# Performance work log

Hardware: AMD Instinct MI355X
Metric: run time of the kernel (lower is better)

The kernel has to match this reference:

```python
import jax, jax.numpy as jnp
import numpy as np

N = 1048576
NUM_LEVELS = 16; LEVEL_DIM = 2; BASE_RES = 16; TABLE = 1 << 19
BOUND = 1.0; DESIRED = 64
_s = np.exp(np.log(DESIRED / BASE_RES) / (NUM_LEVELS - 1))
RESOLUTIONS = [int(np.floor(BASE_RES * _s ** l)) for l in range(NUM_LEVELS)]
OFFS = np.array([[(i >> 0) & 1, (i >> 1) & 1, (i >> 2) & 1] for i in range(8)], dtype=np.int32)
PRIMES = (1, 2654435761, 805459861)


def _corner_index(corner, R):
    # corner: [N,8,3] int32 in [0,R]. Dense index if grid fits in table, else spatial hash.
    if (R + 1) ** 3 <= TABLE:
        stride = jnp.array([1, R + 1, (R + 1) ** 2], dtype=jnp.int32)
        return jnp.sum(corner * stride, axis=-1)
    c = corner.astype(jnp.uint32)
    h = (c[..., 0] * jnp.uint32(PRIMES[0])) ^ (c[..., 1] * jnp.uint32(PRIMES[1])) ^ (c[..., 2] * jnp.uint32(PRIMES[2]))
    return (h % jnp.uint32(TABLE)).astype(jnp.int32)


def hashgrid_encode(x, embeddings):
    # x: [N,3] in [-BOUND,BOUND]; embeddings: [L, TABLE, C]
    pos = (x + BOUND) / (2.0 * BOUND)  # [0,1]
    offs = jnp.asarray(OFFS)  # [8,3]
    outs = []
    for l, R in enumerate(RESOLUTIONS):  # fixed small loop over levels
        xg = pos * R
        x0 = jnp.clip(jnp.floor(xg).astype(jnp.int32), 0, R - 1)  # [N,3]
        f = xg - x0.astype(xg.dtype)  # trilinear fractions [N,3]
        corners = x0[:, None, :] + offs[None]  # [N,8,3]
        idx = _corner_index(corners, R)  # [N,8]
        feats = embeddings[l][idx]  # [N,8,C] irregular gather
        w = jnp.prod(jnp.where(offs[None] == 1, f[:, None, :], 1.0 - f[:, None, :]), axis=-1)  # [N,8]
        outs.append(jnp.sum(feats * w[..., None], axis=1))  # [N,C]
    return jnp.concatenate(outs, axis=-1)  # [N, L*C] = [N,32]


def sh_encode(d):
    # degree-4 real spherical harmonics (16 coeffs), torch-ngp convention
    x, y, z = d[..., 0], d[..., 1], d[..., 2]
    xx, yy, zz = x * x, y * y, z * z
    xy, yz, xz = x * y, y * z, x * z
    return jnp.stack([
        0.28209479177387814 * jnp.ones_like(x),
        -0.48860251190291987 * y,
        0.48860251190291987 * z,
        -0.48860251190291987 * x,
        1.0925484305920792 * xy,
        -1.0925484305920792 * yz,
        0.94617469575755997 * zz - 0.31539156525252005,
        -1.0925484305920792 * xz,
        0.54627421529603959 * (xx - yy),
        0.59004358992664352 * y * (yy - 3.0 * xx),
        2.8906114426405538 * xy * z,
        0.45704579946446572 * y * (1.0 - 5.0 * zz),
        0.3731763325901154 * z * (5.0 * zz - 3.0),
        0.45704579946446572 * x * (1.0 - 5.0 * zz),
        1.4453057213202769 * z * (xx - yy),
        0.59004358992664352 * x * (3.0 * yy - xx),
    ], axis=-1)  # [N,16]


def setup_inputs() -> dict:
    key = jax.random.key(0)
    ks = jax.random.split(key, 8)
    x = jax.random.uniform(ks[0], (N, 3), jnp.float32) * 2.0 - 1.0  # in [-bound, bound]
    d_raw = jax.random.normal(ks[1], (N, 3), jnp.float32)
    d = d_raw / (jnp.linalg.norm(d_raw, axis=-1, keepdims=True) + 1e-8)  # unit view dirs
    embeddings = jax.random.normal(ks[2], (NUM_LEVELS, TABLE, LEVEL_DIM), jnp.float32) * 1e-2
    def w(k, i, o):
        return jax.random.normal(k, (i, o), jnp.float32) / np.sqrt(i).astype(np.float32)
    ws0 = w(ks[3], 32, 64)
    ws1 = w(ks[4], 64, 16)
    wc0 = w(ks[5], 31, 64)
    wc1 = w(ks[6], 64, 64)
    wc2 = w(ks[7], 64, 1)
    return {"x": x, "d": d, "embeddings": embeddings,
            "ws0": ws0, "ws1": ws1, "wc0": wc0, "wc1": wc1, "wc2": wc2}


def reference(x, d, embeddings, ws0, ws1, wc0, wc1, wc2):
    # sigma branch: hashgrid encode -> 2-layer bias-free MLP
    h = hashgrid_encode(x, embeddings)          # [N,32]
    h = jax.nn.relu(h @ ws0) @ ws1              # [N,16]
    sigma = jnp.abs(h[:, :1])                   # [N,1]
    geo_feat = h[:, 1:]                         # [N,15]
    # color branch: SH encode dir, concat geo feature, 3-layer bias-free MLP
    hd = jnp.concatenate([sh_encode(d), geo_feat], axis=-1)  # [N,31]
    c = jax.nn.relu(hd @ wc0)
    c = jax.nn.relu(c @ wc1)
    color = jnp.abs(c @ wc2)                    # [N,1]
    return sigma, color
```

## Files before the change

### kernel.cpp

```cpp
#include <hip/hip_runtime.h>
#include <cmath>

#define NPTS 1048576
#define TABLE_SZ 524288
#define NBUCK 32768

typedef _Float16 half8 __attribute__((ext_vector_type(8)));
typedef _Float16 half4 __attribute__((ext_vector_type(4)));
typedef _Float16 h2 __attribute__((ext_vector_type(2)));
typedef __fp16 fp16x2 __attribute__((ext_vector_type(2)));
typedef float floatx4 __attribute__((ext_vector_type(4)));
typedef unsigned int uint2a4 __attribute__((ext_vector_type(2), aligned(4)));

#define MFMA16x16x32 __builtin_amdgcn_mfma_f32_16x16x32_f16

__device__ __forceinline__ h2 as_h2(unsigned int u) {
    union { unsigned int u; h2 h; } c; c.u = u; return c.h;
}
__device__ __forceinline__ unsigned int pk_u32(float a, float b) {
    union { fp16x2 h; unsigned int u; } c;
    c.h = __builtin_amdgcn_cvt_pkrtz(a, b);
    return c.u;
}

__global__ void prepack_weights(const float* __restrict__ ws0,
                                const float* __restrict__ ws1,
                                const float* __restrict__ wc0,
                                const float* __restrict__ wc1,
                                const float* __restrict__ wc2,
                                half8* __restrict__ wfrag)
{
    const int f = blockIdx.x, l = threadIdx.x;
    const int lane_m = l & 15, k0 = (l >> 4) * 8;
    half8 hv;

    if (f >= 6 && f < 10) {
        const int m = 16*(f-6) + lane_m;
        #pragma unroll
        for (int e = 0; e < 8; ++e) {
            const int k = k0 + e;
            float v;
            if (k < 16)       v = wc0[k*64 + m];
            else if (k == 16) v = 0.0f;
            else              v = wc0[(k-1)*64 + m];
            hv[e] = (_Float16)v;
        }
        wfrag[f*64 + l] = hv;
        return;
    }

    const float* W; int Kreal, Mreal, mt, kt;
    if (f < 4)       { W = ws0; Kreal = 32; Mreal = 64; mt = f;          kt = 0;        }
    else if (f < 6)  { W = ws1; Kreal = 64; Mreal = 16; mt = 0;          kt = f - 4;    }
    else if (f < 18) { W = wc1; Kreal = 64; Mreal = 64; mt = (f-10)>>1;  kt = (f-10)&1; }
    else             { W = wc2; Kreal = 64; Mreal = 1;  mt = 0;          kt = f - 18;   }

    const int m  = 16*mt + lane_m;
    const int kk0 = 32*kt + k0;
    #pragma unroll
    for (int e = 0; e < 8; ++e) {
        const int k = kk0 + e;
        const float v = (m < Mreal && k < Kreal) ? W[k*Mreal + m] : 0.0f;
        hv[e] = (_Float16)v;
    }
    wfrag[f*64 + l] = hv;
}

__global__ __launch_bounds__(256) void convert_tables(
    const float* __restrict__ emb, unsigned int* __restrict__ tabu,
    unsigned int* __restrict__ hist, int zero_hist,
    int4 ra, int4 rb, int4 rc, int4 rd,
    int4 oa, int4 ob, int4 oc, int4 od)
{
    const int l = blockIdx.y;
    if (l == 16) {
        if (zero_hist) {
            const int e = blockIdx.x * 256 + threadIdx.x;
            if (e < NBUCK) hist[e] = 0u;
        }
        return;
    }
    const int q = l >> 2, j = l & 3;
    const int4 rv = (q == 0) ? ra : (q == 1) ? rb : (q == 2) ? rc : rd;
    const int4 ov = (q == 0) ? oa : (q == 1) ? ob : (q == 2) ? oc : od;
    const int R   = (j == 0) ? rv.x : (j == 1) ? rv.y : (j == 2) ? rv.z : rv.w;
    const int off = (j == 0) ? ov.x : (j == 1) ? ov.y : (j == 2) ? ov.z : ov.w;
    const int n = (R+1)*(R+1)*(R+1);
    const int e = blockIdx.x * 256 + threadIdx.x;
    if (e >= n) return;
    const float2 v = *(const float2*)(emb + (size_t)l * (TABLE_SZ*2) + 2*(size_t)e);
    tabu[off + e] = pk_u32(v.x, v.y);
}

__device__ __forceinline__ int bucket_of(float px, float py, float pz) {
    int bx = (int)(px * 32.0f); bx = bx < 0 ? 0 : (bx > 31 ? 31 : bx);
    int by = (int)(py * 32.0f); by = by < 0 ? 0 : (by > 31 ? 31 : by);
    int bz = (int)(pz * 32.0f); bz = bz < 0 ? 0 : (bz > 31 ? 31 : bz);
    return bx | (by << 5) | (bz << 10);
}

__global__ __launch_bounds__(256) void hist_kernel(
    const float* __restrict__ xin, unsigned int* __restrict__ hist,
    unsigned int* __restrict__ rnk)
{
    const int i = blockIdx.x * 256 + threadIdx.x;
    const float px = (xin[3*i+0] + 1.0f) * 0.5f;
    const float py = (xin[3*i+1] + 1.0f) * 0.5f;
    const float pz = (xin[3*i+2] + 1.0f) * 0.5f;
    rnk[i] = atomicAdd(&hist[bucket_of(px, py, pz)], 1u);
}

__global__ __launch_bounds__(1024) void scan_kernel(
    const unsigned int* __restrict__ hist, unsigned int* __restrict__ off)
{
    __shared__ unsigned int ssum[1024];
    const int t = threadIdx.x;
    unsigned int v[32];
    unsigned int s = 0;
    #pragma unroll
    for (int j = 0; j < 32; ++j) {
        const unsigned int h = hist[t*32 + j];
        v[j] = s; s += h;
    }
    ssum[t] = s;
    __syncthreads();
    for (int d = 1; d < 1024; d <<= 1) {
        const unsigned int add = (t >= d) ? ssum[t-d] : 0u;
        __syncthreads();
        ssum[t] += add;
        __syncthreads();
    }
    const unsigned int base = (t == 0) ? 0u : ssum[t-1];
    #pragma unroll
    for (int j = 0; j < 32; ++j) off[t*32 + j] = base + v[j];
}

__global__ __launch_bounds__(256) void scatter_pd(
    const float* __restrict__ xin, const float* __restrict__ din,
    const unsigned int* __restrict__ boff, const unsigned int* __restrict__ rnk,
    float4* __restrict__ pd)
{
    const int i = blockIdx.x * 256 + threadIdx.x;
    const float px = (xin[3*i+0] + 1.0f) * 0.5f;
    const float py = (xin[3*i+1] + 1.0f) * 0.5f;
    const float pz = (xin[3*i+2] + 1.0f) * 0.5f;
    const int b = bucket_of(px, py, pz);
    const unsigned int pos = boff[b] + rnk[i];
    const float dx = din[3*i+0], dy = din[3*i+1], dz = din[3*i+2];
    pd[2*(size_t)pos]     = make_float4(px, py, pz, 0.0f);
    pd[2*(size_t)pos + 1] = make_float4(dx, dy, dz, __uint_as_float((unsigned int)i));
}

__global__ __launch_bounds__(256, 4) void ngp_gather_sorted(
    const float4* __restrict__ pd, const unsigned int* __restrict__ tabu,
    _Float16* __restrict__ feats,
    int4 ra, int4 rb, int4 rc, int4 rd,
    int4 oa, int4 ob, int4 oc, int4 od)
{
    const int p = blockIdx.x * 256 + threadIdx.x;
    const int q = blockIdx.y;

    const float4 xv = pd[2*(size_t)p];
    const float px = xv.x, py = xv.y, pz = xv.z;

    const int4 rv = (q == 0) ? ra : (q == 1) ? rb : (q == 2) ? rc : rd;
    const int4 ov = (q == 0) ? oa : (q == 1) ? ob : (q == 2) ? oc : od;

    uint2a4 P[16];
    float fx[4], fy[4], fz[4];

    #pragma unroll
    for (int j = 0; j < 4; ++j) {
        const int R   = (j == 0) ? rv.x : (j == 1) ? rv.y : (j == 2) ? rv.z : rv.w;
        const int off = (j == 0) ? ov.x : (j == 1) ? ov.y : (j == 2) ? ov.z : ov.w;
        const float Rf = (float)R;
        const float gx = px*Rf, gy = py*Rf, gz = pz*Rf;
        int x0 = (int)floorf(gx); x0 = x0 < 0 ? 0 : (x0 > R-1 ? R-1 : x0);
        int y0 = (int)floorf(gy); y0 = y0 < 0 ? 0 : (y0 > R-1 ? R-1 : y0);
        int z0 = (int)floorf(gz); z0 = z0 < 0 ? 0 : (z0 > R-1 ? R-1 : z0);
        fx[j] = gx - (float)x0; fy[j] = gy - (float)y0; fz[j] = gz - (float)z0;
        const int s1 = R + 1, s2 = s1 * s1;
        const unsigned int* tab = tabu + off;
        const int b = x0 + y0*s1 + z0*s2;
        P[4*j+0] = *(const uint2a4*)(tab + b);
        P[4*j+1] = *(const uint2a4*)(tab + b + s1);
        P[4*j+2] = *(const uint2a4*)(tab + b + s2);
        P[4*j+3] = *(const uint2a4*)(tab + b + s1 + s2);
    }

    union { half8 v; h2 h[4]; } hv;
    #pragma unroll
    for (int j = 0; j < 4; ++j) {
        const _Float16 fxh = (_Float16)fx[j];
        const _Float16 fyh = (_Float16)fy[j];
        const _Float16 fzh = (_Float16)fz[j];
        const h2 fx2 = {fxh, fxh}, fy2 = {fyh, fyh}, fz2 = {fzh, fzh};
        const h2 c000 = as_h2(P[4*j+0].x), c100 = as_h2(P[4*j+0].y);
        const h2 c010 = as_h2(P[4*j+1].x), c110 = as_h2(P[4*j+1].y);
        const h2 c001 = as_h2(P[4*j+2].x), c101 = as_h2(P[4*j+2].y);
        const h2 c011 = as_h2(P[4*j+3].x), c111 = as_h2(P[4*j+3].y);
        const h2 a00 = c000 + fx2 * (c100 - c000);
        const h2 a10 = c010 + fx2 * (c110 - c010);
        const h2 a01 = c001 + fx2 * (c101 - c001);
        const h2 a11 = c011 + fx2 * (c111 - c011);
        const h2 b0  = a00 + fy2 * (a10 - a00);
        const h2 b1  = a01 + fy2 * (a11 - a01);
        hv.h[j] = b0 + fz2 * (b1 - b0);
    }
    *(half8*)&feats[((size_t)q * NPTS + p) * 8] = hv.v;
}

__global__ __launch_bounds__(256, 4) void ngp_gather_lin(
    const float* __restrict__ xin, const unsigned int* __restrict__ tabu,
    _Float16* __restrict__ feats,
    int4 ra, int4 rb, int4 rc, int4 rd,
    int4 oa, int4 ob, int4 oc, int4 od)
{
    const int tid = blockIdx.x * 256 + threadIdx.x;
    const int p = tid >> 2;
    const int q = tid & 3;

    const float px = (xin[3*p+0] + 1.0f) * 0.5f;
    const float py = (xin[3*p+1] + 1.0f) * 0.5f;
    const float pz = (xin[3*p+2] + 1.0f) * 0.5f;

    const int4 rv = (q == 0) ? ra : (q == 1) ? rb : (q == 2) ? rc : rd;
    const int4 ov = (q == 0) ? oa : (q == 1) ? ob : (q == 2) ? oc : od;

    uint2a4 P[16];
    float fx[4], fy[4], fz[4];
    #pragma unroll
    for (int j = 0; j < 4; ++j) {
        const int R   = (j == 0) ? rv.x : (j == 1) ? rv.y : (j == 2) ? rv.z : rv.w;
        const int off = (j == 0) ? ov.x : (j == 1) ? ov.y : (j == 2) ? ov.z : ov.w;
        const float Rf = (float)R;
        const float gx = px*Rf, gy = py*Rf, gz = pz*Rf;
        int x0 = (int)floorf(gx); x0 = x0 < 0 ? 0 : (x0 > R-1 ? R-1 : x0);
        int y0 = (int)floorf(gy); y0 = y0 < 0 ? 0 : (y0 > R-1 ? R-1 : y0);
        int z0 = (int)floorf(gz); z0 = z0 < 0 ? 0 : (z0 > R-1 ? R-1 : z0);
        fx[j] = gx - (float)x0; fy[j] = gy - (float)y0; fz[j] = gz - (float)z0;
        const int s1 = R + 1, s2 = s1 * s1;
        const unsigned int* tab = tabu + off;
        const int b = x0 + y0*s1 + z0*s2;
        P[4*j+0] = *(const uint2a4*)(tab + b);
        P[4*j+1] = *(const uint2a4*)(tab + b + s1);
        P[4*j+2] = *(const uint2a4*)(tab + b + s2);
        P[4*j+3] = *(const uint2a4*)(tab + b + s1 + s2);
    }
    union { half8 v; h2 h[4]; } hv;
    #pragma unroll
    for (int j = 0; j < 4; ++j) {
        const _Float16 fxh = (_Float16)fx[j];
        const _Float16 fyh = (_Float16)fy[j];
        const _Float16 fzh = (_Float16)fz[j];
        const h2 fx2 = {fxh, fxh}, fy2 = {fyh, fyh}, fz2 = {fzh, fzh};
        const h2 c000 = as_h2(P[4*j+0].x), c100 = as_h2(P[4*j+0].y);
        const h2 c010 = as_h2(P[4*j+1].x), c110 = as_h2(P[4*j+1].y);
        const h2 c001 = as_h2(P[4*j+2].x), c101 = as_h2(P[4*j+2].y);
        const h2 c011 = as_h2(P[4*j+3].x), c111 = as_h2(P[4*j+3].y);
        const h2 a00 = c000 + fx2 * (c100 - c000);
        const h2 a10 = c010 + fx2 * (c110 - c010);
        const h2 a01 = c001 + fx2 * (c101 - c001);
        const h2 a11 = c011 + fx2 * (c111 - c011);
        const h2 b0  = a00 + fy2 * (a10 - a00);
        const h2 b1  = a01 + fy2 * (a11 - a01);
        hv.h[j] = b0 + fz2 * (b1 - b0);
    }
    *(half8*)&feats[(size_t)p*32 + q*8] = hv.v;
}

template<int MODE>
__global__ __launch_bounds__(256) void ngp_mlp(
    const float* __restrict__ din, const _Float16* __restrict__ feats,
    const float4* __restrict__ pd,
    const half8* __restrict__ wfrag, float* __restrict__ out)
{
    __shared__ __align__(16) _Float16 smM[4][64][72];

    const int tid  = threadIdx.x;
    const int w    = tid >> 6, lane = tid & 63;
    const int gbase = (blockIdx.x * 4 + w) * 64;

    const int n = lane & 15, g = lane >> 4;
    const floatx4 zz = {0.f, 0.f, 0.f, 0.f};

    unsigned int orig[4];
    float dX[4], dY[4], dZ[4];
    #pragma unroll
    for (int nt = 0; nt < 4; ++nt) {
        const int pt = nt*16 + n;
        if (MODE == 2) {
            const float4 dv = pd[2*(size_t)(gbase + pt) + 1];
            dX[nt] = dv.x; dY[nt] = dv.y; dZ[nt] = dv.z;
            orig[nt] = __float_as_uint(dv.w);
        } else {
            orig[nt] = gbase + pt;
            dX[nt] = din[3*orig[nt]+0]; dY[nt] = din[3*orig[nt]+1]; dZ[nt] = din[3*orig[nt]+2];
        }
    }

    auto storeQ = [&](int pt, int mt, floatx4 a) {
        union { unsigned int u[2]; half4 v; } c;
        c.u[0] = pk_u32(fmaxf(a[0], 0.f), fmaxf(a[1], 0.f));
        c.u[1] = pk_u32(fmaxf(a[2], 0.f), fmaxf(a[3], 0.f));
        *(half4*)&smM[w][pt][16*mt + 4*g] = c.v;
    };

    {
        const half8 A0 = wfrag[0*64+lane], A1 = wfrag[1*64+lane];
        const half8 A2 = wfrag[2*64+lane], A3 = wfrag[3*64+lane];
        #pragma unroll
        for (int nt = 0; nt < 4; ++nt) {
            const int pt = nt*16 + n;
            half8 B;
            if (MODE == 2)
                B = *(const half8*)&feats[((size_t)g * NPTS + (gbase + pt)) * 8];
            else
                B = *(const half8*)&feats[(size_t)(gbase + pt)*32 + 8*g];
            floatx4 a0 = MFMA16x16x32(A0, B, zz, 0,0,0);
            floatx4 a1 = MFMA16x16x32(A1, B, zz, 0,0,0);
            floatx4 a2 = MFMA16x16x32(A2, B, zz, 0,0,0);
            floatx4 a3 = MFMA16x16x32(A3, B, zz, 0,0,0);
            storeQ(pt, 0, a0); storeQ(pt, 1, a1); storeQ(pt, 2, a2); storeQ(pt, 3, a3);
        }
    }
    asm volatile("" ::: "memory");

    unsigned int s1a[4], s1b[4];
    {
        const half8 A0 = wfrag[4*64+lane], A1 = wfrag[5*64+lane];
        #pragma unroll
        for (int nt = 0; nt < 4; ++nt) {
            const int pt = nt*16 + n;
            const half8 B0 = *(const half8*)&smM[w][pt][ 0 + 8*g];
            const half8 B1 = *(const half8*)&smM[w][pt][32 + 8*g];
            floatx4 acc = MFMA16x16x32(A0, B0, zz, 0,0,0);
            acc = MFMA16x16x32(A1, B1, acc, 0,0,0);
            s1a[nt] = pk_u32(acc[0], acc[1]);
            s1b[nt] = pk_u32(acc[2], acc[3]);
            if (g == 0) out[orig[nt]] = fabsf(acc[0]);
        }
    }
    asm volatile("" ::: "memory");

    {
        const half8 A0 = wfrag[6*64+lane], A1 = wfrag[7*64+lane];
        const half8 A2 = wfrag[8*64+lane], A3 = wfrag[9*64+lane];
        const int srcA = ((g & 1) << 5) + n;
        #pragma unroll
        for (int nt = 0; nt < 4; ++nt) {
            const int pt = nt*16 + n;
            const unsigned int w0 = __shfl(s1a[nt], srcA);
            const unsigned int w1 = __shfl(s1b[nt], srcA);
            const unsigned int w2 = __shfl(s1a[nt], srcA + 16);
            const unsigned int w3 = __shfl(s1b[nt], srcA + 16);
            union { half8 v; unsigned int u[4]; } B;
            if (g < 2) {
                const float x = dX[nt], y = dY[nt], z = dZ[nt];
                const float xx = x*x, yy = y*y, zzq = z*z;
                const float xy = x*y, yz = y*z, xz = x*z;
                float s[8];
                if (g == 0) {
                    s[0] = 0.28209479177387814f;
                    s[1] = -0.48860251190291987f * y;
                    s[2] =  0.48860251190291987f * z;
                    s[3] = -0.48860251190291987f * x;
                    s[4] =  1.0925484305920792f * xy;
                    s[5] = -1.0925484305920792f * yz;
                    s[6] =  0.94617469575756f * zzq - 0.31539156525252005f;
                    s[7] = -1.0925484305920792f * xz;
                } else {
                    s[0] =  0.5462742152960396f * (xx - yy);
                    s[1] =  0.5900435899266435f * y * (yy - 3.0f*xx);
                    s[2] =  2.890611442640554f * xy * z;
                    s[3] =  0.4570457994644657f * y * (1.0f - 5.0f*zzq);
                    s[4] =  0.3731763325901154f * z * (5.0f*zzq - 3.0f);
                    s[5] =  0.4570457994644657f * x * (1.0f - 5.0f*zzq);
                    s[6] =  1.445305721320277f * z * (xx - yy);
                    s[7] =  0.5900435899266435f * x * (3.0f*yy - xx);
                }
                B.u[0] = pk_u32(s[0], s[1]); B.u[1] = pk_u32(s[2], s[3]);
                B.u[2] = pk_u32(s[4], s[5]); B.u[3] = pk_u32(s[6], s[7]);
            } else {
                B.u[0] = w0; B.u[1] = w1; B.u[2] = w2; B.u[3] = w3;
            }
            floatx4 a0 = MFMA16x16x32(A0, B.v, zz, 0,0,0);
            floatx4 a1 = MFMA16x16x32(A1, B.v, zz, 0,0,0);
            floatx4 a2 = MFMA16x16x32(A2, B.v, zz, 0,0,0);
            floatx4 a3 = MFMA16x16x32(A3, B.v, zz, 0,0,0);
            storeQ(pt, 0, a0); storeQ(pt, 1, a1); storeQ(pt, 2, a2); storeQ(pt, 3, a3);
        }
    }
    asm volatile("" ::: "memory");

    {
        const half8 A0 = wfrag[10*64+lane], A1 = wfrag[11*64+lane];
        const half8 A2 = wfrag[12*64+lane], A3 = wfrag[13*64+lane];
        const half8 A4 = wfrag[14*64+lane], A5 = wfrag[15*64+lane];
        const half8 A6 = wfrag[16*64+lane], A7 = wfrag[17*64+lane];
        #pragma unroll
        for (int nt = 0; nt < 4; ++nt) {
            const int pt = nt*16 + n;
            const half8 B0 = *(const half8*)&smM[w][pt][ 0 + 8*g];
            const half8 B1 = *(const half8*)&smM[w][pt][32 + 8*g];
            floatx4 a0 = MFMA16x16x32(A0, B0, zz, 0,0,0); a0 = MFMA16x16x32(A1, B1, a0, 0,0,0);
            floatx4 a1 = MFMA16x16x32(A2, B0, zz, 0,0,0); a1 = MFMA16x16x32(A3, B1, a1, 0,0,0);
            floatx4 a2 = MFMA16x16x32(A4, B0, zz, 0,0,0); a2 = MFMA16x16x32(A5, B1, a2, 0,0,0);
            floatx4 a3 = MFMA16x16x32(A6, B0, zz, 0,0,0); a3 = MFMA16x16x32(A7, B1, a3, 0,0,0);
            storeQ(pt, 0, a0); storeQ(pt, 1, a1); storeQ(pt, 2, a2); storeQ(pt, 3, a3);
        }
    }
    asm volatile("" ::: "memory");

    {
        const half8 A0 = wfrag[18*64+lane], A1 = wfrag[19*64+lane];
        #pragma unroll
        for (int nt = 0; nt < 4; ++nt) {
            const int pt = nt*16 + n;
            const half8 B0 = *(const half8*)&smM[w][pt][ 0 + 8*g];
            const half8 B1 = *(const half8*)&smM[w][pt][32 + 8*g];
            floatx4 acc = MFMA16x16x32(A0, B0, zz, 0,0,0);
            acc = MFMA16x16x32(A1, B1, acc, 0,0,0);
            if (g == 0) out[NPTS + orig[nt]] = fabsf(acc[0]);
        }
    }
}

extern "C" void kernel_launch(void* const* d_in, const int* in_sizes, int n_in,
                              void* d_out, int out_size, void* d_ws, size_t ws_size,
                              hipStream_t stream)
{
    const float* x   = (const float*)d_in[0];
    const float* d   = (const float*)d_in[1];
    const float* emb = (const float*)d_in[2];
    const float* ws0 = (const float*)d_in[3];
    const float* ws1 = (const float*)d_in[4];
    const float* wc0 = (const float*)d_in[5];
    const float* wc1 = (const float*)d_in[6];
    const float* wc2 = (const float*)d_in[7];
    float* out = (float*)d_out;

    const size_t OFF_WFRAG = 0;
    const size_t OFF_TABU  = 32768;
    const size_t OFF_FEATS = OFF_TABU + 8388608;
    const size_t OFF_RNK   = OFF_FEATS;
    const size_t OFF_HIST  = OFF_FEATS + 67108864;
    const size_t OFF_BOFF  = OFF_HIST + NBUCK*4;
    const size_t OFF_PD    = OFF_BOFF + NBUCK*4;
    const size_t NEED_SORT = OFF_PD + (size_t)NPTS*32;
    const size_t NEED_LIN  = OFF_HIST;

    half8* wfrag        = (half8*)((char*)d_ws + OFF_WFRAG);
    unsigned int* tabu  = (unsigned int*)((char*)d_ws + OFF_TABU);
    _Float16* feats     = (_Float16*)((char*)d_ws + OFF_FEATS);
    unsigned int* rnk   = (unsigned int*)((char*)d_ws + OFF_RNK);
    unsigned int* hist  = (unsigned int*)((char*)d_ws + OFF_HIST);
    unsigned int* boff  = (unsigned int*)((char*)d_ws + OFF_BOFF);
    float4* pd          = (float4*)((char*)d_ws + OFF_PD);

    int r[16], off[16];
    const double s = std::exp(std::log(4.0) / 15.0);
    int acc = 0;
    for (int l = 0; l < 16; ++l) {
        r[l] = (int)std::floor(16.0 * std::pow(s, (double)l));
        off[l] = acc;
        acc += (r[l]+1)*(r[l]+1)*(r[l]+1);
    }
    const int4 ra = {r[0],  r[1],  r[2],  r[3]};
    const int4 rb = {r[4],  r[5],  r[6],  r[7]};
    const int4 rc = {r[8],  r[9],  r[10], r[11]};
    const int4 rd = {r[12], r[13], r[14], r[15]};
    const int4 oa = {off[0],  off[1],  off[2],  off[3]};
    const int4 ob = {off[4],  off[5],  off[6],  off[7]};
    const int4 oc = {off[8],  off[9],  off[10], off[11]};
    const int4 od = {off[12], off[13], off[14], off[15]};

    prepack_weights<<<20, 64, 0, stream>>>(ws0, ws1, wc0, wc1, wc2, wfrag);

    const int nmax = (r[15]+1)*(r[15]+1)*(r[15]+1);
    dim3 cgrid((nmax + 255) / 256, 17);

    if (ws_size >= NEED_SORT) {
        convert_tables<<<cgrid, 256, 0, stream>>>(emb, tabu, hist, 1, ra, rb, rc, rd, oa, ob, oc, od);
        hist_kernel<<<NPTS/256, 256, 0, stream>>>(x, hist, rnk);
        scan_kernel<<<1, 1024, 0, stream>>>(hist, boff);
        scatter_pd<<<NPTS/256, 256, 0, stream>>>(x, d, boff, rnk, pd);
        dim3 ggrid(NPTS/256, 4);
        ngp_gather_sorted<<<ggrid, 256, 0, stream>>>(pd, tabu, feats, ra, rb, rc, rd, oa, ob, oc, od);
        ngp_mlp<2><<<NPTS/256, 256, 0, stream>>>(d, feats, pd, wfrag, out);
    } else if (ws_size >= NEED_LIN) {
        convert_tables<<<cgrid, 256, 0, stream>>>(emb, tabu, hist, 0, ra, rb, rc, rd, oa, ob, oc, od);
        ngp_gather_lin<<<NPTS*4/256, 256, 0, stream>>>(x, tabu, feats, ra, rb, rc, rd, oa, ob, oc, od);
        ngp_mlp<0><<<NPTS/256, 256, 0, stream>>>(d, feats, nullptr, wfrag, out);
    }
}
```

Measured before the change: 183.5 us.

## Fuse sorted hashgrid gather into MLP kernel via shared-memory features

Merges the sorted-path gather kernel into the MLP kernel. Each wave gathers one group of four levels for all 256 points in the block and writes the features into shared memory, so the 64 MB fp16 feature buffer is no longer written to and read back from global memory. The cost is that gather and MLP phases now share one block's occupancy: the old (256,4) launch bound on the gather is gone and each wave runs serial gather iterations, which may reduce latency hiding for the random table loads.

```diff
diff --git a/kernel.cpp b/kernel.cpp
--- a/kernel.cpp
+++ b/kernel.cpp
@@ -151,153 +151,91 @@
     pd[2*(size_t)pos + 1] = make_float4(dx, dy, dz, __uint_as_float((unsigned int)i));
 }
 
-__global__ __launch_bounds__(256, 4) void ngp_gather_sorted(
+__global__ __launch_bounds__(256) void ngp_fused_sorted(
     const float4* __restrict__ pd, const unsigned int* __restrict__ tabu,
-    _Float16* __restrict__ feats,
+    const half8* __restrict__ wfrag, float* __restrict__ out,
     int4 ra, int4 rb, int4 rc, int4 rd,
     int4 oa, int4 ob, int4 oc, int4 od)
 {
-    const int p = blockIdx.x * 256 + threadIdx.x;
-    const int q = blockIdx.y;
-
-    const float4 xv = pd[2*(size_t)p];
-    const float px = xv.x, py = xv.y, pz = xv.z;
-
-    const int4 rv = (q == 0) ? ra : (q == 1) ? rb : (q == 2) ? rc : rd;
-    const int4 ov = (q == 0) ? oa : (q == 1) ? ob : (q == 2) ? oc : od;
-
-    uint2a4 P[16];
-    float fx[4], fy[4], fz[4];
-
-    #pragma unroll
-    for (int j = 0; j < 4; ++j) {
-        const int R   = (j == 0) ? rv.x : (j == 1) ? rv.y : (j == 2) ? rv.z : rv.w;
-        const int off = (j == 0) ? ov.x : (j == 1) ? ov.y : (j == 2) ? ov.z : ov.w;
-        const float Rf = (float)R;
-        const float gx = px*Rf, gy = py*Rf, gz = pz*Rf;
-        int x0 = (int)floorf(gx); x0 = x0 < 0 ? 0 : (x0 > R-1 ? R-1 : x0);
-        int y0 = (int)floorf(gy); y0 = y0 < 0 ? 0 : (y0 > R-1 ? R-1 : y0);
-        int z0 = (int)floorf(gz); z0 = z0 < 0 ? 0 : (z0 > R-1 ? R-1 : z0);
-        fx[j] = gx - (float)x0; fy[j] = gy - (float)y0; fz[j] = gz - (float)z0;
-        const int s1 = R + 1, s2 = s1 * s1;
-        const unsigned int* tab = tabu + off;
-        const int b = x0 + y0*s1 + z0*s2;
-        P[4*j+0] = *(const uint2a4*)(tab + b);
-        P[4*j+1] = *(const uint2a4*)(tab + b + s1);
-        P[4*j+2] = *(const uint2a4*)(tab + b + s2);
-        P[4*j+3] = *(const uint2a4*)(tab + b + s1 + s2);
-    }
-
-    union { half8 v; h2 h[4]; } hv;
-    #pragma unroll
-    for (int j = 0; j < 4; ++j) {
-        const _Float16 fxh = (_Float16)fx[j];
-        const _Float16 fyh = (_Float16)fy[j];
-        const _Float16 fzh = (_Float16)fz[j];
-        const h2 fx2 = {fxh, fxh}, fy2 = {fyh, fyh}, fz2 = {fzh, fzh};
-        const h2 c000 = as_h2(P[4*j+0].x), c100 = as_h2(P[4*j+0].y);
-        const h2 c010 = as_h2(P[4*j+1].x), c110 = as_h2(P[4*j+1].y);
-        const h2 c001 = as_h2(P[4*j+2].x), c101 = as_h2(P[4*j+2].y);
-        const h2 c011 = as_h2(P[4*j+3].x), c111 = as_h2(P[4*j+3].y);
-        const h2 a00 = c000 + fx2 * (c100 - c000);
-        const h2 a10 = c010 + fx2 * (c110 - c010);
-        const h2 a01 = c001 + fx2 * (c101 - c001);
-        const h2 a11 = c011 + fx2 * (c111 - c011);
-        const h2 b0  = a00 + fy2 * (a10 - a00);
-        const h2 b1  = a01 + fy2 * (a11 - a01);
-        hv.h[j] = b0 + fz2 * (b1 - b0);
-    }
-    *(half8*)&feats[((size_t)q * NPTS + p) * 8] = hv.v;
-}
-
-__global__ __launch_bounds__(256, 4) void ngp_gather_lin(
-    const float* __restrict__ xin, const unsigned int* __restrict__ tabu,
-    _Float16* __restrict__ feats,
-    int4 ra, int4 rb, int4 rc, int4 rd,
-    int4 oa, int4 ob, int4 oc, int4 od)
-{
-    const int tid = blockIdx.x * 256 + threadIdx.x;
-    const int p = tid >> 2;
-    const int q = tid & 3;
-
-    const float px = (xin[3*p+0] + 1.0f) * 0.5f;
-    const float py = (xin[3*p+1] + 1.0f) * 0.5f;
-    const float pz = (xin[3*p+2] + 1.0f) * 0.5f;
-
-    const int4 rv = (q == 0) ? ra : (q == 1) ? rb : (q == 2) ? rc : rd;
-    const int4 ov = (q == 0) ? oa : (q == 1) ? ob : (q == 2) ? oc : od;
-
-    uint2a4 P[16];
-    float fx[4], fy[4], fz[4];
-    #pragma unroll
-    for (int j = 0; j < 4; ++j) {
-        const int R   = (j == 0) ? rv.x : (j == 1) ? rv.y : (j == 2) ? rv.z : rv.w;
-        const int off = (j == 0) ? ov.x : (j == 1) ? ov.y : (j == 2) ? ov.z : ov.w;
-        const float Rf = (float)R;
-        const float gx = px*Rf, gy = py*Rf, gz = pz*Rf;
-        int x0 = (int)floorf(gx); x0 = x0 < 0 ? 0 : (x0 > R-1 ? R-1 : x0);
-        int y0 = (int)floorf(gy); y0 = y0 < 0 ? 0 : (y0 > R-1 ? R-1 : y0);
-        int z0 = (int)floorf(gz); z0 = z0 < 0 ? 0 : (z0 > R-1 ? R-1 : z0);
-        fx[j] = gx - (float)x0; fy[j] = gy - (float)y0; fz[j] = gz - (float)z0;
-        const int s1 = R + 1, s2 = s1 * s1;
-        const unsigned int* tab = tabu + off;
-        const int b = x0 + y0*s1 + z0*s2;
-        P[4*j+0] = *(const uint2a4*)(tab + b);
-        P[4*j+1] = *(const uint2a4*)(tab + b + s1);
-        P[4*j+2] = *(const uint2a4*)(tab + b + s2);
-        P[4*j+3] = *(const uint2a4*)(tab + b + s1 + s2);
-    }
-    union { half8 v; h2 h[4]; } hv;
-    #pragma unroll
-    for (int j = 0; j < 4; ++j) {
-        const _Float16 fxh = (_Float16)fx[j];
-        const _Float16 fyh = (_Float16)fy[j];
-        const _Float16 fzh = (_Float16)fz[j];
-        const h2 fx2 = {fxh, fxh}, fy2 = {fyh, fyh}, fz2 = {fzh, fzh};
-        const h2 c000 = as_h2(P[4*j+0].x), c100 = as_h2(P[4*j+0].y);
-        const h2 c010 = as_h2(P[4*j+1].x), c110 = as_h2(P[4*j+1].y);
-        const h2 c001 = as_h2(P[4*j+2].x), c101 = as_h2(P[4*j+2].y);
-        const h2 c011 = as_h2(P[4*j+3].x), c111 = as_h2(P[4*j+3].y);
-        const h2 a00 = c000 + fx2 * (c100 - c000);
-        const h2 a10 = c010 + fx2 * (c110 - c010);
-        const h2 a01 = c001 + fx2 * (c101 - c001);
-        const h2 a11 = c011 + fx2 * (c111 - c011);
-        const h2 b0  = a00 + fy2 * (a10 - a00);
-        const h2 b1  = a01 + fy2 * (a11 - a01);
-        hv.h[j] = b0 + fz2 * (b1 - b0);
-    }
-    *(half8*)&feats[(size_t)p*32 + q*8] = hv.v;
-}
-
-template<int MODE>
-__global__ __launch_bounds__(256) void ngp_mlp(
-    const float* __restrict__ din, const _Float16* __restrict__ feats,
-    const float4* __restrict__ pd,
-    const half8* __restrict__ wfrag, float* __restrict__ out)
-{
     __shared__ __align__(16) _Float16 smM[4][64][72];
+    _Float16* fls = (_Float16*)smM;
 
     const int tid  = threadIdx.x;
     const int w    = tid >> 6, lane = tid & 63;
-    const int gbase = (blockIdx.x * 4 + w) * 64;
-
+    const int pblock = blockIdx.x * 256;
     const int n = lane & 15, g = lane >> 4;
+    const int gbase = pblock + w * 64;
     const floatx4 zz = {0.f, 0.f, 0.f, 0.f};
 
     unsigned int orig[4];
     float dX[4], dY[4], dZ[4];
     #pragma unroll
     for (int nt = 0; nt < 4; ++nt) {
-        const int pt = nt*16 + n;
-        if (MODE == 2) {
-            const float4 dv = pd[2*(size_t)(gbase + pt) + 1];
-            dX[nt] = dv.x; dY[nt] = dv.y; dZ[nt] = dv.z;
-            orig[nt] = __float_as_uint(dv.w);
-        } else {
-            orig[nt] = gbase + pt;
-            dX[nt] = din[3*orig[nt]+0]; dY[nt] = din[3*orig[nt]+1]; dZ[nt] = din[3*orig[nt]+2];
-        }
-    }
+        const float4 dv = pd[2*(size_t)(gbase + nt*16 + n) + 1];
+        dX[nt] = dv.x; dY[nt] = dv.y; dZ[nt] = dv.z;
+        orig[nt] = __float_as_uint(dv.w);
+    }
+
+    {
+        const int q = w;
+        const int4 rv = (q == 0) ? ra : (q == 1) ? rb : (q == 2) ? rc : rd;
+        const int4 ov = (q == 0) ? oa : (q == 1) ? ob : (q == 2) ? oc : od;
+        #pragma unroll 2
+        for (int it = 0; it < 4; ++it) {
+            const int pl = it*64 + lane;
+            const float4 xv = pd[2*(size_t)(pblock + pl)];
+            const float px = xv.x, py = xv.y, pz = xv.z;
+
+            uint2a4 P[16];
+            float fx[4], fy[4], fz[4];
+            #pragma unroll
+            for (int j = 0; j < 4; ++j) {
+                const int R   = (j == 0) ? rv.x : (j == 1) ? rv.y : (j == 2) ? rv.z : rv.w;
+                const int off = (j == 0) ? ov.x : (j == 1) ? ov.y : (j == 2) ? ov.z : ov.w;
+                const float Rf = (float)R;
+                const float gx = px*Rf, gy = py*Rf, gz = pz*Rf;
+                int x0 = (int)floorf(gx); x0 = x0 < 0 ? 0 : (x0 > R-1 ? R-1 : x0);
+                int y0 = (int)floorf(gy); y0 = y0 < 0 ? 0 : (y0 > R-1 ? R-1 : y0);
+                int z0 = (int)floorf(gz); z0 = z0 < 0 ? 0 : (z0 > R-1 ? R-1 : z0);
+                fx[j] = gx - (float)x0; fy[j] = gy - (float)y0; fz[j] = gz - (float)z0;
+                const int s1 = R + 1, s2 = s1 * s1;
+                const unsigned int* tab = tabu + off;
+                const int b = x0 + y0*s1 + z0*s2;
+                P[4*j+0] = *(const uint2a4*)(tab + b);
+                P[4*j+1] = *(const uint2a4*)(tab + b + s1);
+                P[4*j+2] = *(const uint2a4*)(tab + b + s2);
+                P[4*j+3] = *(const uint2a4*)(tab + b + s1 + s2);
+            }
+
+            union { half8 v; h2 h[4]; } hv;
+            #pragma unroll
+            for (int j = 0; j < 4; ++j) {
+                const _Float16 fxh = (_Float16)fx[j];
+                const _Float16 fyh = (_Float16)fy[j];
+                const _Float16 fzh = (_Float16)fz[j];
+                const h2 fx2 = {fxh, fxh}, fy2 = {fyh, fyh}, fz2 = {fzh, fzh};
+                const h2 c000 = as_h2(P[4*j+0].x), c100 = as_h2(P[4*j+0].y);
+                const h2 c010 = as_h2(P[4*j+1].x), c110 = as_h2(P[4*j+1].y);
+                const h2 c001 = as_h2(P[4*j+2].x), c101 = as_h2(P[4*j+2].y);
+                const h2 c011 = as_h2(P[4*j+3].x), c111 = as_h2(P[4*j+3].y);
+                const h2 a00 = c000 + fx2 * (c100 - c000);
+                const h2 a10 = c010 + fx2 * (c110 - c010);
+                const h2 a01 = c001 + fx2 * (c101 - c001);
+                const h2 a11 = c011 + fx2 * (c111 - c011);
+                const h2 b0  = a00 + fy2 * (a10 - a00);
+                const h2 b1  = a01 + fy2 * (a11 - a01);
+                hv.h[j] = b0 + fz2 * (b1 - b0);
+            }
+            *(half8*)&fls[(size_t)pl*40 + q*8] = hv.v;
+        }
+    }
+    __syncthreads();
+
+    half8 B0s[4];
+    #pragma unroll
+    for (int nt = 0; nt < 4; ++nt)
+        B0s[nt] = *(const half8*)&fls[(size_t)(w*64 + nt*16 + n)*40 + g*8];
+    __syncthreads();
 
     auto storeQ = [&](int pt, int mt, floatx4 a) {
         union { unsigned int u[2]; half4 v; } c;
@@ -312,11 +250,7 @@
         #pragma unroll
         for (int nt = 0; nt < 4; ++nt) {
             const int pt = nt*16 + n;
-            half8 B;
-            if (MODE == 2)
-                B = *(const half8*)&feats[((size_t)g * NPTS + (gbase + pt)) * 8];
-            else
-                B = *(const half8*)&feats[(size_t)(gbase + pt)*32 + 8*g];
+            const half8 B = B0s[nt];
             floatx4 a0 = MFMA16x16x32(A0, B, zz, 0,0,0);
             floatx4 a1 = MFMA16x16x32(A1, B, zz, 0,0,0);
             floatx4 a2 = MFMA16x16x32(A2, B, zz, 0,0,0);
@@ -426,6 +360,209 @@
     }
 }
 
+__global__ __launch_bounds__(256, 4) void ngp_gather_lin(
+    const float* __restrict__ xin, const unsigned int* __restrict__ tabu,
+    _Float16* __restrict__ feats,
+    int4 ra, int4 rb, int4 rc, int4 rd,
+    int4 oa, int4 ob, int4 oc, int4 od)
+{
+    const int tid = blockIdx.x * 256 + threadIdx.x;
+    const int p = tid >> 2;
+    const int q = tid & 3;
+
+    const float px = (xin[3*p+0] + 1.0f) * 0.5f;
+    const float py = (xin[3*p+1] + 1.0f) * 0.5f;
+    const float pz = (xin[3*p+2] + 1.0f) * 0.5f;
+
+    const int4 rv = (q == 0) ? ra : (q == 1) ? rb : (q == 2) ? rc : rd;
+    const int4 ov = (q == 0) ? oa : (q == 1) ? ob : (q == 2) ? oc : od;
+
+    uint2a4 P[16];
+    float fx[4], fy[4], fz[4];
+    #pragma unroll
+    for (int j = 0; j < 4; ++j) {
+        const int R   = (j == 0) ? rv.x : (j == 1) ? rv.y : (j == 2) ? rv.z : rv.w;
+        const int off = (j == 0) ? ov.x : (j == 1) ? ov.y : (j == 2) ? ov.z : ov.w;
+        const float Rf = (float)R;
+        const float gx = px*Rf, gy = py*Rf, gz = pz*Rf;
+        int x0 = (int)floorf(gx); x0 = x0 < 0 ? 0 : (x0 > R-1 ? R-1 : x0);
+        int y0 = (int)floorf(gy); y0 = y0 < 0 ? 0 : (y0 > R-1 ? R-1 : y0);
+        int z0 = (int)floorf(gz); z0 = z0 < 0 ? 0 : (z0 > R-1 ? R-1 : z0);
+        fx[j] = gx - (float)x0; fy[j] = gy - (float)y0; fz[j] = gz - (float)z0;
+        const int s1 = R + 1, s2 = s1 * s1;
+        const unsigned int* tab = tabu + off;
+        const int b = x0 + y0*s1 + z0*s2;
+        P[4*j+0] = *(const uint2a4*)(tab + b);
+        P[4*j+1] = *(const uint2a4*)(tab + b + s1);
+        P[4*j+2] = *(const uint2a4*)(tab + b + s2);
+        P[4*j+3] = *(const uint2a4*)(tab + b + s1 + s2);
+    }
+    union { half8 v; h2 h[4]; } hv;
+    #pragma unroll
+    for (int j = 0; j < 4; ++j) {
+        const _Float16 fxh = (_Float16)fx[j];
+        const _Float16 fyh = (_Float16)fy[j];
+        const _Float16 fzh = (_Float16)fz[j];
+        const h2 fx2 = {fxh, fxh}, fy2 = {fyh, fyh}, fz2 = {fzh, fzh};
+        const h2 c000 = as_h2(P[4*j+0].x), c100 = as_h2(P[4*j+0].y);
+        const h2 c010 = as_h2(P[4*j+1].x), c110 = as_h2(P[4*j+1].y);
+        const h2 c001 = as_h2(P[4*j+2].x), c101 = as_h2(P[4*j+2].y);
+        const h2 c011 = as_h2(P[4*j+3].x), c111 = as_h2(P[4*j+3].y);
+        const h2 a00 = c000 + fx2 * (c100 - c000);
+        const h2 a10 = c010 + fx2 * (c110 - c010);
+        const h2 a01 = c001 + fx2 * (c101 - c001);
+        const h2 a11 = c011 + fx2 * (c111 - c011);
+        const h2 b0  = a00 + fy2 * (a10 - a00);
+        const h2 b1  = a01 + fy2 * (a11 - a01);
+        hv.h[j] = b0 + fz2 * (b1 - b0);
+    }
+    *(half8*)&feats[(size_t)p*32 + q*8] = hv.v;
+}
+
+__global__ __launch_bounds__(256) void ngp_mlp_lin(
+    const float* __restrict__ din, const _Float16* __restrict__ feats,
+    const half8* __restrict__ wfrag, float* __restrict__ out)
+{
+    __shared__ __align__(16) _Float16 smM[4][64][72];
+
+    const int tid  = threadIdx.x;
+    const int w    = tid >> 6, lane = tid & 63;
+    const int gbase = (blockIdx.x * 4 + w) * 64;
+
+    const int n = lane & 15, g = lane >> 4;
+    const floatx4 zz = {0.f, 0.f, 0.f, 0.f};
+
+    unsigned int orig[4];
+    float dX[4], dY[4], dZ[4];
+    #pragma unroll
+    for (int nt = 0; nt < 4; ++nt) {
+        orig[nt] = gbase + nt*16 + n;
+        dX[nt] = din[3*orig[nt]+0]; dY[nt] = din[3*orig[nt]+1]; dZ[nt] = din[3*orig[nt]+2];
+    }
+
+    auto storeQ = [&](int pt, int mt, floatx4 a) {
+        union { unsigned int u[2]; half4 v; } c;
+        c.u[0] = pk_u32(fmaxf(a[0], 0.f), fmaxf(a[1], 0.f));
+        c.u[1] = pk_u32(fmaxf(a[2], 0.f), fmaxf(a[3], 0.f));
+        *(half4*)&smM[w][pt][16*mt + 4*g] = c.v;
+    };
+
+    {
+        const half8 A0 = wfrag[0*64+lane], A1 = wfrag[1*64+lane];
+        const half8 A2 = wfrag[2*64+lane], A3 = wfrag[3*64+lane];
+        #pragma unroll
+        for (int nt = 0; nt < 4; ++nt) {
+            const int pt = nt*16 + n;
+            const half8 B = *(const half8*)&feats[(size_t)(gbase + pt)*32 + 8*g];
+            floatx4 a0 = MFMA16x16x32(A0, B, zz, 0,0,0);
+            floatx4 a1 = MFMA16x16x32(A1, B, zz, 0,0,0);
+            floatx4 a2 = MFMA16x16x32(A2, B, zz, 0,0,0);
+            floatx4 a3 = MFMA16x16x32(A3, B, zz, 0,0,0);
+            storeQ(pt, 0, a0); storeQ(pt, 1, a1); storeQ(pt, 2, a2); storeQ(pt, 3, a3);
+        }
+    }
+    asm volatile("" ::: "memory");
+
+    unsigned int s1a[4], s1b[4];
+    {
+        const half8 A0 = wfrag[4*64+lane], A1 = wfrag[5*64+lane];
+        #pragma unroll
+        for (int nt = 0; nt < 4; ++nt) {
+            const int pt = nt*16 + n;
+            const half8 B0 = *(const half8*)&smM[w][pt][ 0 + 8*g];
+            const half8 B1 = *(const half8*)&smM[w][pt][32 + 8*g];
+            floatx4 acc = MFMA16x16x32(A0, B0, zz, 0,0,0);
+            acc = MFMA16x16x32(A1, B1, acc, 0,0,0);
+            s1a[nt] = pk_u32(acc[0], acc[1]);
+            s1b[nt] = pk_u32(acc[2], acc[3]);
+            if (g == 0) out[orig[nt]] = fabsf(acc[0]);
+        }
+    }
+    asm volatile("" ::: "memory");
+
+    {
+        const half8 A0 = wfrag[6*64+lane], A1 = wfrag[7*64+lane];
+        const half8 A2 = wfrag[8*64+lane], A3 = wfrag[9*64+lane];
+        const int srcA = ((g & 1) << 5) + n;
+        #pragma unroll
+        for (int nt = 0; nt < 4; ++nt) {
+            const int pt = nt*16 + n;
+            const unsigned int w0 = __shfl(s1a[nt], srcA);
+            const unsigned int w1 = __shfl(s1b[nt], srcA);
+            const unsigned int w2 = __shfl(s1a[nt], srcA + 16);
+            const unsigned int w3 = __shfl(s1b[nt], srcA + 16);
+            union { half8 v; unsigned int u[4]; } B;
+            if (g < 2) {
+                const float x = dX[nt], y = dY[nt], z = dZ[nt];
+                const float xx = x*x, yy = y*y, zzq = z*z;
+                const float xy = x*y, yz = y*z, xz = x*z;
+                float s[8];
+                if (g == 0) {
+                    s[0] = 0.28209479177387814f;
+                    s[1] = -0.48860251190291987f * y;
+                    s[2] =  0.48860251190291987f * z;
+                    s[3] = -0.48860251190291987f * x;
+                    s[4] =  1.0925484305920792f * xy;
+                    s[5] = -1.0925484305920792f * yz;
+                    s[6] =  0.94617469575756f * zzq - 0.31539156525252005f;
+                    s[7] = -1.0925484305920792f * xz;
+                } else {
+                    s[0] =  0.5462742152960396f * (xx - yy);
+                    s[1] =  0.5900435899266435f * y * (yy - 3.0f*xx);
+                    s[2] =  2.890611442640554f * xy * z;
+                    s[3] =  0.4570457994644657f * y * (1.0f - 5.0f*zzq);
+                    s[4] =  0.3731763325901154f * z * (5.0f*zzq - 3.0f);
+                    s[5] =  0.4570457994644657f * x * (1.0f - 5.0f*zzq);
+                    s[6] =  1.445305721320277f * z * (xx - yy);
+                    s[7] =  0.5900435899266435f * x * (3.0f*yy - xx);
+                }
+                B.u[0] = pk_u32(s[0], s[1]); B.u[1] = pk_u32(s[2], s[3]);
+                B.u[2] = pk_u32(s[4], s[5]); B.u[3] = pk_u32(s[6], s[7]);
+            } else {
+                B.u[0] = w0; B.u[1] = w1; B.u[2] = w2; B.u[3] = w3;
+            }
+            floatx4 a0 = MFMA16x16x32(A0, B.v, zz, 0,0,0);
+            floatx4 a1 = MFMA16x16x32(A1, B.v, zz, 0,0,0);
+            floatx4 a2 = MFMA16x16x32(A2, B.v, zz, 0,0,0);
+            floatx4 a3 = MFMA16x16x32(A3, B.v, zz, 0,0,0);
+            storeQ(pt, 0, a0); storeQ(pt, 1, a1); storeQ(pt, 2, a2); storeQ(pt, 3, a3);
+        }
+    }
+    asm volatile("" ::: "memory");
+
+    {
+        const half8 A0 = wfrag[10*64+lane], A1 = wfrag[11*64+lane];
+        const half8 A2 = wfrag[12*64+lane], A3 = wfrag[13*64+lane];
+        const half8 A4 = wfrag[14*64+lane], A5 = wfrag[15*64+lane];
+        const half8 A6 = wfrag[16*64+lane], A7 = wfrag[17*64+lane];
+        #pragma unroll
+        for (int nt = 0; nt < 4; ++nt) {
+            const int pt = nt*16 + n;
+            const half8 B0 = *(const half8*)&smM[w][pt][ 0 + 8*g];
+            const half8 B1 = *(const half8*)&smM[w][pt][32 + 8*g];
+            floatx4 a0 = MFMA16x16x32(A0, B0, zz, 0,0,0); a0 = MFMA16x16x32(A1, B1, a0, 0,0,0);
+            floatx4 a1 = MFMA16x16x32(A2, B0, zz, 0,0,0); a1 = MFMA16x16x32(A3, B1, a1, 0,0,0);
+            floatx4 a2 = MFMA16x16x32(A4, B0, zz, 0,0,0); a2 = MFMA16x16x32(A5, B1, a2, 0,0,0);
+            floatx4 a3 = MFMA16x16x32(A6, B0, zz, 0,0,0); a3 = MFMA16x16x32(A7, B1, a3, 0,0,0);
+            storeQ(pt, 0, a0); storeQ(pt, 1, a1); storeQ(pt, 2, a2); storeQ(pt, 3, a3);
+        }
+    }
+    asm volatile("" ::: "memory");
+
+    {
+        const half8 A0 = wfrag[18*64+lane], A1 = wfrag[19*64+lane];
+        #pragma unroll
+        for (int nt = 0; nt < 4; ++nt) {
+            const int pt = nt*16 + n;
+            const half8 B0 = *(const half8*)&smM[w][pt][ 0 + 8*g];
+            const half8 B1 = *(const half8*)&smM[w][pt][32 + 8*g];
+            floatx4 acc = MFMA16x16x32(A0, B0, zz, 0,0,0);
+            acc = MFMA16x16x32(A1, B1, acc, 0,0,0);
+            if (g == 0) out[NPTS + orig[nt]] = fabsf(acc[0]);
+        }
+    }
+}
+
 extern "C" void kernel_launch(void* const* d_in, const int* in_sizes, int n_in,
                               void* d_out, int out_size, void* d_ws, size_t ws_size,
                               hipStream_t stream)
@@ -442,21 +579,21 @@
 
     const size_t OFF_WFRAG = 0;
     const size_t OFF_TABU  = 32768;
-    const size_t OFF_FEATS = OFF_TABU + 8388608;
-    const size_t OFF_RNK   = OFF_FEATS;
-    const size_t OFF_HIST  = OFF_FEATS + 67108864;
+    const size_t OFF_RNK   = OFF_TABU + 8388608;
+    const size_t OFF_HIST  = OFF_RNK + 4194304;
     const size_t OFF_BOFF  = OFF_HIST + NBUCK*4;
     const size_t OFF_PD    = OFF_BOFF + NBUCK*4;
     const size_t NEED_SORT = OFF_PD + (size_t)NPTS*32;
-    const size_t NEED_LIN  = OFF_HIST;
+    const size_t OFF_FEATS = OFF_RNK;
+    const size_t NEED_LIN  = OFF_FEATS + (size_t)NPTS*64;
 
     half8* wfrag        = (half8*)((char*)d_ws + OFF_WFRAG);
     unsigned int* tabu  = (unsigned int*)((char*)d_ws + OFF_TABU);
-    _Float16* feats     = (_Float16*)((char*)d_ws + OFF_FEATS);
     unsigned int* rnk   = (unsigned int*)((char*)d_ws + OFF_RNK);
     unsigned int* hist  = (unsigned int*)((char*)d_ws + OFF_HIST);
     unsigned int* boff  = (unsigned int*)((char*)d_ws + OFF_BOFF);
     float4* pd          = (float4*)((char*)d_ws + OFF_PD);
+    _Float16* feats     = (_Float16*)((char*)d_ws + OFF_FEATS);
 
     int r[16], off[16];
     const double s = std::exp(std::log(4.0) / 15.0);
@@ -485,12 +622,10 @@
         hist_kernel<<<NPTS/256, 256, 0, stream>>>(x, hist, rnk);
         scan_kernel<<<1, 1024, 0, stream>>>(hist, boff);
         scatter_pd<<<NPTS/256, 256, 0, stream>>>(x, d, boff, rnk, pd);
-        dim3 ggrid(NPTS/256, 4);
-        ngp_gather_sorted<<<ggrid, 256, 0, stream>>>(pd, tabu, feats, ra, rb, rc, rd, oa, ob, oc, od);
-        ngp_mlp<2><<<NPTS/256, 256, 0, stream>>>(d, feats, pd, wfrag, out);
+        ngp_fused_sorted<<<NPTS/256, 256, 0, stream>>>(pd, tabu, wfrag, out, ra, rb, rc, rd, oa, ob, oc, od);
     } else if (ws_size >= NEED_LIN) {
         convert_tables<<<cgrid, 256, 0, stream>>>(emb, tabu, hist, 0, ra, rb, rc, rd, oa, ob, oc, od);
         ngp_gather_lin<<<NPTS*4/256, 256, 0, stream>>>(x, tabu, feats, ra, rb, rc, rd, oa, ob, oc, od);
-        ngp_mlp<0><<<NPTS/256, 256, 0, stream>>>(d, feats, nullptr, wfrag, out);
-    }
-}
+        ngp_mlp_lin<<<NPTS/256, 256, 0, stream>>>(d, feats, wfrag, out);
+    }
+}
```

New measurement: 171.1 us (median of 2 runs). -6.7%, faster.
